# Kernel optimization log

Measured on AMD Instinct MI355X. Metric: run time of the kernel, lower is better.

The kernel has to match this reference:

```python
import jax, jax.numpy as jnp
import numpy as np

B, L, DIM, DQK = 4, 8192, 512, 512
THRESH = 0.5
TARGET_N = 6.0
RATIO_W = 0.03
LR_DIFF = 0.75
EPS = 1e-8


def setup_inputs() -> dict:
    key = jax.random.key(0)
    k1, k2, k3 = jax.random.split(key, 3)
    tokens = jax.random.normal(k1, (B, L, DIM), dtype=jnp.float32)
    # Linear(dim, 2*dqk, bias=False) weight, torch layout [out, in]
    Wqk = jax.random.normal(k2, (2 * DQK, DIM), dtype=jnp.float32) / np.sqrt(DIM).astype(np.float32)
    start_key = jax.random.normal(k3, (DQK,), dtype=jnp.float32) * 0.01  # heads=1
    return {"tokens": tokens, "Wqk": Wqk, "start_key": start_key}


def _straight_through(t, value):
    return t + jax.lax.stop_gradient(value - t)


def _frac_gradient(t, frac):
    # forward = t, backward grad scaled by frac
    return _straight_through(t * frac, t)


def _cosine_sim(a, b):
    dot = jnp.sum(a * b, axis=-1)
    na = jnp.maximum(jnp.sqrt(jnp.sum(a * a, axis=-1)), EPS)
    nb = jnp.maximum(jnp.sqrt(jnp.sum(b * b, axis=-1)), EPS)
    return dot / (na * nb)


def _assoc_scan(gates, x):
    # h_t = gates_t * h_{t-1} + x_t along axis 1 (inclusive first-order scan)
    def comb(l, r):
        al, bl = l
        ar, br = r
        return al * ar, br + ar * bl
    _, h = jax.lax.associative_scan(comb, (gates[..., None], x), axis=1)
    return h


def reference(tokens, Wqk, start_key):
    Bn, Ln, D = tokens.shape
    qk = jnp.einsum('bnd,ed->bne', tokens, Wqk)          # [B, L, 2*DQK]
    queries, keys = qk[..., :DQK], qk[..., DQK:]
    # key for position i is key_{i-1}, with learned start key at position 0
    keys_shift = jnp.concatenate(
        [jnp.broadcast_to(start_key, (Bn, 1, DQK)), keys[:, :-1]], axis=1)
    cos = _cosine_sim(queries, keys_shift)               # [B, L]
    probs = (1.0 - cos) * 0.5
    boundary = (probs > THRESH).at[:, 0].set(True)       # [B, L] bool
    num_chunks = boundary.sum(axis=-1)                   # [B]

    # stable compaction: boundary positions first, in order
    order = jnp.argsort(jnp.logical_not(boundary).astype(jnp.int32), axis=1)  # [B, L]
    ar = jnp.arange(Ln)
    chunk_mask = ar[None, :] < num_chunks[:, None]       # valid chunk slots
    pos = jnp.where(chunk_mask, order, Ln)               # boundary positions, sentinel L
    next_pos = jnp.concatenate([pos[:, 1:], jnp.full((Bn, 1), Ln, dtype=pos.dtype)], axis=1)
    chunk_lens = jnp.where(chunk_mask, next_pos - pos, 0)  # [B, L] int

    gathered = jnp.take_along_axis(tokens, order[..., None], axis=1)  # [B, L, D]
    boundary_probs = jnp.where(chunk_mask, jnp.take_along_axis(probs, order, axis=1), 0.0)
    gates = 1.0 - boundary_probs                         # padded slots -> 1 (matches torch, never read)
    downsampled = gathered * boundary_probs[..., None]   # padded slots -> 0

    confidence = jnp.where(boundary, probs, 1.0 - probs)
    scale = _straight_through(confidence, 1.0)           # forward value 1.0

    # aux ratio loss (with straight-through soft boundary fraction)
    Nt = TARGET_N
    F_hard = boundary.astype(probs.dtype)
    F_soft = jax.nn.sigmoid(probs - THRESH)
    F = _straight_through(F_soft, F_hard)
    Gm = probs.mean(axis=-1)
    Fm = F.mean(axis=-1)
    aux = (Nt / (Nt - 1.0)) * ((Nt - 1.0) * Fm * Gm + (1.0 - Fm) * (1.0 - Gm))
    weighted_aux_loss = aux.mean() * RATIO_W

    downsampled_out = _frac_gradient(downsampled, 1.0 / LR_DIFF)

    # ---- upsample path (the returned closure in the torch module) ----
    scanned = _assoc_scan(gates, downsampled_out)        # smooth across chunks
    rank = jnp.cumsum(boundary.astype(jnp.int32), axis=1) - 1  # chunk id of each token
    upsampled = jnp.take_along_axis(scanned, rank[..., None], axis=1)  # [B, L, D]
    upsampled = upsampled * scale[..., None]
    upsampled = _frac_gradient(upsampled, LR_DIFF)

    return downsampled_out, upsampled, weighted_aux_loss
```

## Files before the change

### kernel.cpp

```cpp
#include <hip/hip_runtime.h>
#include <cstdint>
#include <cstddef>

#define L 8192
#define BATCH 4
#define DQK 512
#define M_TOT (BATCH*L)
#define EPSC 1e-8f

typedef __attribute__((ext_vector_type(8))) short bf16x8;
typedef __attribute__((ext_vector_type(4))) float f32x4;
typedef __attribute__((ext_vector_type(8))) unsigned short u16x8;

__device__ __forceinline__ unsigned short bf16_rne(float x) {
  union { float f; unsigned u; } v; v.f = x;
  unsigned r = v.u + 0x7fffu + ((v.u >> 16) & 1u);
  return (unsigned short)(r >> 16);
}
__device__ __forceinline__ float bf16_tof(unsigned short b) {
  union { unsigned u; float f; } v; v.u = ((unsigned)b) << 16;
  return v.f;
}
__device__ __forceinline__ void gload_lds16(const void* g, void* l) {
  __builtin_amdgcn_global_load_lds(
      (const __attribute__((address_space(1))) unsigned int*)g,
      (__attribute__((address_space(3))) unsigned int*)l, 16, 0, 0);
}

__global__ __launch_bounds__(256) void k_split(const float* __restrict__ tokens,
                                               const float* __restrict__ Wqk,
                                               unsigned short* __restrict__ A1,
                                               unsigned short* __restrict__ A2,
                                               unsigned short* __restrict__ A3,
                                               unsigned short* __restrict__ W1,
                                               unsigned short* __restrict__ W2,
                                               unsigned short* __restrict__ W3) {
  const float* src; unsigned short *d1, *d2, *d3; size_t e0;
  if (blockIdx.x < 8192) {
    src = tokens; d1 = A1; d2 = A2; d3 = A3;
    e0 = ((size_t)blockIdx.x * 256 + threadIdx.x) * 8;
  } else {
    src = Wqk; d1 = W1; d2 = W2; d3 = W3;
    e0 = ((size_t)(blockIdx.x - 8192) * 256 + threadIdx.x) * 8;
  }
  float v[8];
  *(float4*)&v[0] = *(const float4*)(src + e0);
  *(float4*)&v[4] = *(const float4*)(src + e0 + 4);
  unsigned short o1[8], o2[8], o3[8];
  #pragma unroll
  for (int j = 0; j < 8; ++j) {
    float x = v[j];
    unsigned short b1 = bf16_rne(x);
    float r1 = x - bf16_tof(b1);
    unsigned short b2 = bf16_rne(r1);
    float r2 = r1 - bf16_tof(b2);
    unsigned short b3 = bf16_rne(r2);
    o1[j] = b1; o2[j] = b2; o3[j] = b3;
  }
  *(u16x8*)(d1 + e0) = *(u16x8*)o1;
  *(u16x8*)(d2 + e0) = *(u16x8*)o2;
  *(u16x8*)(d3 + e0) = *(u16x8*)o3;
}

__global__ __launch_bounds__(256, 3) void k_gemm_bf16(
    const unsigned short* __restrict__ A1, const unsigned short* __restrict__ A2,
    const unsigned short* __restrict__ A3,
    const unsigned short* __restrict__ W1, const unsigned short* __restrict__ W2,
    const unsigned short* __restrict__ W3,
    float* __restrict__ C) {
  __shared__ unsigned short lds[6 * 512 * 8];
  const int g = (blockIdx.x & 7) * 256 + (blockIdx.x >> 3);
  const int bx = g & 7;
  const int by = g >> 3;
  const int t = threadIdx.x;
  const int lane = t & 63;
  const int w = t >> 6;
  const int wr = w >> 1, wc = w & 1;

  f32x4 acc[4][4];
  #pragma unroll
  for (int i = 0; i < 4; ++i)
    #pragma unroll
    for (int j = 0; j < 4; ++j) acc[i][j] = (f32x4){0.f, 0.f, 0.f, 0.f};

  const unsigned short* srcA[3] = {A1, A2, A3};
  const unsigned short* srcW[3] = {W1, W2, W3};
  const int arow = by * 128;
  const int wrow = bx * 128;
  const int kg = lane >> 4;
  const int fr = lane & 15;

  for (int ks = 0; ks < 16; ++ks) {
    __syncthreads();
    const int kofs = ks * 32;
    #pragma unroll
    for (int s = 0; s < 3; ++s) {
      #pragma unroll
      for (int it = 0; it < 2; ++it) {
        const int p = it * 256 + t;
        const int row = p & 127, pg = p >> 7;
        gload_lds16(srcA[s] + (size_t)(arow + row) * 512 + kofs + pg * 8,
                    &lds[(s * 512 + p) * 8]);
        gload_lds16(srcW[s] + (size_t)(wrow + row) * 512 + kofs + pg * 8,
                    &lds[((3 + s) * 512 + p) * 8]);
      }
    }
    __syncthreads();

    bf16x8 bfr[4][3];
    #pragma unroll
    for (int nf = 0; nf < 4; ++nf) {
      const int row = wc * 64 + nf * 16 + fr;
      #pragma unroll
      for (int s = 0; s < 3; ++s)
        bfr[nf][s] = *(const bf16x8*)&lds[(((3 + s) * 512) + kg * 128 + row) * 8];
    }
    #pragma unroll
    for (int mf = 0; mf < 4; ++mf) {
      const int row = wr * 64 + mf * 16 + fr;
      bf16x8 a1 = *(const bf16x8*)&lds[((0 * 512) + kg * 128 + row) * 8];
      bf16x8 a2 = *(const bf16x8*)&lds[((1 * 512) + kg * 128 + row) * 8];
      bf16x8 a3 = *(const bf16x8*)&lds[((2 * 512) + kg * 128 + row) * 8];
      #pragma unroll
      for (int nf = 0; nf < 4; ++nf) {
        f32x4 c = acc[mf][nf];
        c = __builtin_amdgcn_mfma_f32_16x16x32_bf16(a1, bfr[nf][0], c, 0, 0, 0);
        c = __builtin_amdgcn_mfma_f32_16x16x32_bf16(a1, bfr[nf][1], c, 0, 0, 0);
        c = __builtin_amdgcn_mfma_f32_16x16x32_bf16(a2, bfr[nf][0], c, 0, 0, 0);
        c = __builtin_amdgcn_mfma_f32_16x16x32_bf16(a2, bfr[nf][1], c, 0, 0, 0);
        c = __builtin_amdgcn_mfma_f32_16x16x32_bf16(a1, bfr[nf][2], c, 0, 0, 0);
        c = __builtin_amdgcn_mfma_f32_16x16x32_bf16(a3, bfr[nf][0], c, 0, 0, 0);
        acc[mf][nf] = c;
      }
    }
  }
  const int fq = lane >> 4;
  #pragma unroll
  for (int mf = 0; mf < 4; ++mf) {
    #pragma unroll
    for (int nf = 0; nf < 4; ++nf) {
      const int col = bx * 128 + wc * 64 + nf * 16 + fr;
      #pragma unroll
      for (int r = 0; r < 4; ++r) {
        const int rrow = by * 128 + wr * 64 + mf * 16 + fq * 4 + r;
        C[(size_t)rrow * 1024 + col] = acc[mf][nf][r];
      }
    }
  }
}

__global__ __launch_bounds__(256) void k_gemm(const float* __restrict__ A,
                                              const float* __restrict__ W,
                                              float* __restrict__ C) {
  __shared__ float As[8][128];
  __shared__ float Bs[8][128];
  const int bx = blockIdx.x & 7;
  const int by = blockIdx.x >> 3;
  const int t  = threadIdx.x;
  const int tx = t & 15, ty = t >> 4;
  const int lr = t >> 1;
  const int lc = (t & 1) * 4;
  const float* Ag = A + (size_t)(by*128 + lr)*512 + lc;
  const float* Wg = W + (size_t)(bx*128 + lr)*512 + lc;
  float acc[8][8];
  #pragma unroll
  for (int i=0;i<8;i++)
    #pragma unroll
    for (int j=0;j<8;j++) acc[i][j]=0.f;

  for (int k0 = 0; k0 < 512; k0 += 8) {
    float4 av = *(const float4*)(Ag + k0);
    float4 bv = *(const float4*)(Wg + k0);
    __syncthreads();
    As[lc+0][lr]=av.x; As[lc+1][lr]=av.y; As[lc+2][lr]=av.z; As[lc+3][lr]=av.w;
    Bs[lc+0][lr]=bv.x; Bs[lc+1][lr]=bv.y; Bs[lc+2][lr]=bv.z; Bs[lc+3][lr]=bv.w;
    __syncthreads();
    #pragma unroll
    for (int kk=0;kk<8;kk++) {
      float af[8], bf[8];
      *(float4*)&af[0] = *(const float4*)&As[kk][ty*8];
      *(float4*)&af[4] = *(const float4*)&As[kk][ty*8+4];
      *(float4*)&bf[0] = *(const float4*)&Bs[kk][tx*8];
      *(float4*)&bf[4] = *(const float4*)&Bs[kk][tx*8+4];
      #pragma unroll
      for (int i=0;i<8;i++)
        #pragma unroll
        for (int j=0;j<8;j++)
          acc[i][j] = fmaf(af[i], bf[j], acc[i][j]);
    }
  }
  const int crow = by*128 + ty*8;
  const int ccol = bx*128 + tx*8;
  #pragma unroll
  for (int i=0;i<8;i++) {
    float* cp = C + (size_t)(crow+i)*1024 + ccol;
    *(float4*)cp     = make_float4(acc[i][0],acc[i][1],acc[i][2],acc[i][3]);
    *(float4*)(cp+4) = make_float4(acc[i][4],acc[i][5],acc[i][6],acc[i][7]);
  }
}

__global__ __launch_bounds__(256) void k_cos(const float* __restrict__ qk,
                                             const float* __restrict__ start_key,
                                             float* __restrict__ probs) {
  const int wid = threadIdx.x >> 6;
  const int lane = threadIdx.x & 63;
  const int p = blockIdx.x*4 + wid;
  const int n = p & (L-1);
  const float* q  = qk + (size_t)p*1024;
  const float* ks = (n==0) ? start_key : (qk + (size_t)(p-1)*1024 + 512);
  float dot=0.f, nq=0.f, nk=0.f;
  const int e0 = lane*8;
  #pragma unroll
  for (int j=0;j<8;j+=4) {
    float4 qv = *(const float4*)(q+e0+j);
    float4 kv = *(const float4*)(ks+e0+j);
    dot = fmaf(qv.x,kv.x,dot); dot = fmaf(qv.y,kv.y,dot);
    dot = fmaf(qv.z,kv.z,dot); dot = fmaf(qv.w,kv.w,dot);
    nq  = fmaf(qv.x,qv.x,nq);  nq  = fmaf(qv.y,qv.y,nq);
    nq  = fmaf(qv.z,qv.z,nq);  nq  = fmaf(qv.w,qv.w,nq);
    nk  = fmaf(kv.x,kv.x,nk);  nk  = fmaf(kv.y,kv.y,nk);
    nk  = fmaf(kv.z,kv.z,nk);  nk  = fmaf(kv.w,kv.w,nk);
  }
  #pragma unroll
  for (int m=32;m>=1;m>>=1) {
    dot += __shfl_xor(dot,m);
    nq  += __shfl_xor(nq,m);
    nk  += __shfl_xor(nk,m);
  }
  if (lane==0) {
    float na = fmaxf(sqrtf(nq), EPSC);
    float nb = fmaxf(sqrtf(nk), EPSC);
    float c  = dot/(na*nb);
    probs[p] = 0.5f*(1.f - c);
  }
}

__global__ __launch_bounds__(1024) void k_scan_bd(const float* __restrict__ probs,
                                                  int* __restrict__ bpos,
                                                  int* __restrict__ num_chunks,
                                                  float* __restrict__ auxvals) {
  const int b = blockIdx.x;
  const float* pb = probs + b*L;
  const int t = threadIdx.x;
  float pv[8]; int bd[8];
  const int base = t*8;
  float psum=0.f; int cnt=0;
  #pragma unroll
  for (int j=0;j<8;j++) {
    pv[j] = pb[base+j];
    bd[j] = (base+j == 0) || (pv[j] > 0.5f);
    cnt += bd[j];
    psum += pv[j];
  }
  const int lane = t & 63, w = t >> 6;
  int x = cnt;
  #pragma unroll
  for (int off=1; off<64; off<<=1) {
    int y = __shfl_up(x, off);
    if (lane >= off) x += y;
  }
  float ps = psum;
  #pragma unroll
  for (int m=32;m>=1;m>>=1) ps += __shfl_xor(ps, m);
  __shared__ int wsum[16]; __shared__ int wpre[17]; __shared__ float fsum[16];
  if (lane == 63) wsum[w] = x;
  if (lane == 0)  fsum[w] = ps;
  __syncthreads();
  if (t == 0) {
    int run = 0; float tot = 0.f;
    for (int i=0;i<16;i++) { wpre[i] = run; run += wsum[i]; tot += fsum[i]; }
    wpre[16] = run;
    num_chunks[b] = run;
    float Gm = tot / (float)L;
    float Fm = (float)run / (float)L;
    auxvals[b] = 1.2f * (5.f*Fm*Gm + (1.f-Fm)*(1.f-Gm));
  }
  __syncthreads();
  int rank = wpre[w] + (x - cnt);
  #pragma unroll
  for (int j=0;j<8;j++) {
    if (bd[j]) { bpos[b*L + rank] = base + j; rank++; }
  }
}

__global__ __launch_bounds__(512) void k_scan_local(const float* __restrict__ tokens,
                                                    const float* __restrict__ probs,
                                                    const int* __restrict__ bpos,
                                                    const int* __restrict__ num_chunks,
                                                    float* __restrict__ local_h,
                                                    float* __restrict__ gpref,
                                                    float* __restrict__ hend,
                                                    float* __restrict__ Pseg,
                                                    float* __restrict__ down) {
  const int b = blockIdx.x >> 6;
  const int s = blockIdx.x & 63;
  const int c = threadIdx.x;
  const int nc = num_chunks[b];
  const int i0 = s*128;
  const int seg = b*64 + s;
  const int z0 = (i0 > nc) ? i0 : nc;
  for (int i = z0; i < i0 + 128; ++i)
    down[((size_t)(b*L + i))*512 + c] = 0.f;
  if (i0 >= nc) {
    hend[(size_t)seg*512 + c] = 0.f;
    if (c==0) Pseg[seg] = 1.f;
    return;
  }
  const int iend = (i0+128 < nc) ? i0+128 : nc;
  const int cntc = iend - i0;
  __shared__ float p_s[128];
  __shared__ int n_s[128];
  if (c < cntc) {
    int n = bpos[b*L + i0 + c];
    n_s[c] = n;
    p_s[c] = probs[b*L + n];
  }
  __syncthreads();
  float h = 0.f, gp = 1.f;
  for (int i = i0; i < iend; ++i) {
    const int ii = i - i0;
    const float p = p_s[ii];
    const float g = 1.f - p;
    const float x = tokens[((size_t)(b*L + n_s[ii]))*512 + c] * p;
    h = fmaf(g, h, x);
    gp *= g;
    down[((size_t)(b*L + i))*512 + c] = x;
    local_h[((size_t)(b*L + i))*512 + c] = h;
    if (c==0) gpref[b*L + i] = gp;
  }
  hend[(size_t)seg*512 + c] = h;
  if (c==0) Pseg[seg] = gp;
}

__global__ __launch_bounds__(512) void k_seg_combine(const float* __restrict__ hend,
                                                     const float* __restrict__ Pseg,
                                                     float* __restrict__ carry_in) {
  const int b = blockIdx.x;
  const int c = threadIdx.x;
  float carry = 0.f;
  for (int s = 0; s < 64; ++s) {
    const int seg = b*64 + s;
    carry_in[(size_t)seg*512 + c] = carry;
    carry = fmaf(Pseg[seg], carry, hend[(size_t)seg*512 + c]);
  }
}

__global__ __launch_bounds__(512) void k_expand(const float* __restrict__ local_h,
                                                const float* __restrict__ gpref,
                                                const float* __restrict__ carry_in,
                                                const int* __restrict__ bpos,
                                                const int* __restrict__ num_chunks,
                                                float* __restrict__ up) {
  const int b = blockIdx.x >> 6;
  const int s = blockIdx.x & 63;
  const int c = threadIdx.x;
  const int nc = num_chunks[b];
  const int i0 = s*128;
  if (i0 >= nc) return;
  const int iend = (i0+128 < nc) ? i0+128 : nc;
  const int cntc = iend - i0;
  __shared__ int n_s[129];
  __shared__ float gp_s[128];
  if (c < cntc) { n_s[c] = bpos[b*L + i0 + c]; gp_s[c] = gpref[b*L + i0 + c]; }
  if (c == 0)   n_s[cntc] = (iend < nc) ? bpos[b*L + iend] : L;
  __syncthreads();
  const float carry = carry_in[((size_t)(b*64 + s))*512 + c];
  for (int i = i0; i < iend; ++i) {
    const int ii = i - i0;
    const float hf = fmaf(gp_s[ii], carry, local_h[((size_t)(b*L + i))*512 + c]);
    const int n0 = n_s[ii], n1 = n_s[ii+1];
    for (int n = n0; n < n1; ++n)
      up[((size_t)(b*L + n))*512 + c] = hf;
  }
}

__global__ void k_final(const float* __restrict__ auxvals, float* __restrict__ outp) {
  outp[0] = (auxvals[0]+auxvals[1]+auxvals[2]+auxvals[3]) * 0.25f * 0.03f;
}

extern "C" void kernel_launch(void* const* d_in, const int* in_sizes, int n_in,
                              void* d_out, int out_size, void* d_ws, size_t ws_size,
                              hipStream_t stream) {
  const float* tokens    = (const float*)d_in[0];
  const float* Wqk       = (const float*)d_in[1];
  const float* start_key = (const float*)d_in[2];
  float* out  = (float*)d_out;
  float* down = out;
  float* up   = out + (size_t)M_TOT*512;
  float* qk   = out;

  char* ws = (char*)d_ws;
  const size_t A_BYTES = (size_t)M_TOT*512*2;
  const size_t W_BYTES = (size_t)1024*512*2;
  const size_t STAGED_BASE = 3*A_BYTES + 3*W_BYTES;
  const size_t SMALL_BYTES = (size_t)M_TOT*4*3 + (size_t)BATCH*64*512*4*2
                           + (size_t)BATCH*64*4 + BATCH*4*2 + 256;
  const bool staged = ws_size >= STAGED_BASE + SMALL_BYTES;

  unsigned short* A1 = (unsigned short*)ws;
  unsigned short* A2 = (unsigned short*)(ws + A_BYTES);
  unsigned short* A3 = (unsigned short*)(ws + 2*A_BYTES);
  unsigned short* W1 = (unsigned short*)(ws + 3*A_BYTES);
  unsigned short* W2 = (unsigned short*)(ws + 3*A_BYTES + W_BYTES);
  unsigned short* W3 = (unsigned short*)(ws + 3*A_BYTES + 2*W_BYTES);

  float* local_h = (float*)ws;
  size_t off = staged ? STAGED_BASE : (size_t)M_TOT*512*4;
  float* probs    = (float*)(ws + off); off += (size_t)M_TOT*4;
  int*   bpos     = (int*)  (ws + off); off += (size_t)M_TOT*4;
  float* gpref    = (float*)(ws + off); off += (size_t)M_TOT*4;
  float* hend     = (float*)(ws + off); off += (size_t)BATCH*64*512*4;
  float* carry_in = (float*)(ws + off); off += (size_t)BATCH*64*512*4;
  float* Pseg     = (float*)(ws + off); off += (size_t)BATCH*64*4;
  int*   num_chunks = (int*)(ws + off); off += (size_t)BATCH*4;
  float* auxvals  = (float*)(ws + off); off += (size_t)BATCH*4;

  if (staged) {
    k_split<<<8448, 256, 0, stream>>>(tokens, Wqk, A1, A2, A3, W1, W2, W3);
    k_gemm_bf16<<<2048, 256, 0, stream>>>(A1, A2, A3, W1, W2, W3, qk);
  } else {
    k_gemm<<<2048, 256, 0, stream>>>(tokens, Wqk, qk);
  }
  k_cos<<<M_TOT/4, 256, 0, stream>>>(qk, start_key, probs);
  k_scan_bd<<<BATCH, 1024, 0, stream>>>(probs, bpos, num_chunks, auxvals);
  k_scan_local<<<BATCH*64, 512, 0, stream>>>(tokens, probs, bpos, num_chunks,
                                             local_h, gpref, hend, Pseg, down);
  k_seg_combine<<<BATCH, 512, 0, stream>>>(hend, Pseg, carry_in);
  k_expand<<<BATCH*64, 512, 0, stream>>>(local_h, gpref, carry_in, bpos, num_chunks, up);
  k_final<<<1, 1, 0, stream>>>(auxvals, out + (size_t)2*M_TOT*512);
}
```

Measured before the change: 411.4 us.

## Recompute local scan in expand instead of storing local_h; parallel segment carry scan

The local scan kernel no longer writes the per-position local_h and gpref arrays. The expand kernel instead rescans each segment from its carry-in, re-reading down and probs. The serial per-batch segment combine is replaced by a parallel Hillis-Steele scan over segments, and segments shrink from 128 to 64 chunks so there are twice as many blocks. This removes a full [B,L,512] write and re-read of local_h, at the cost of re-reading down, a serial recurrence inside expand, and some extra memory traffic for the larger hend/carry arrays.

```diff
diff --git a/kernel.cpp b/kernel.cpp
--- a/kernel.cpp
+++ b/kernel.cpp
@@ -6,6 +6,8 @@
 #define BATCH 4
 #define DQK 512
 #define M_TOT (BATCH*L)
+#define NSEG 128
+#define SEGC 64
 #define EPSC 1e-8f
 
 typedef __attribute__((ext_vector_type(8))) short bf16x8;
@@ -287,29 +289,27 @@
                                                     const float* __restrict__ probs,
                                                     const int* __restrict__ bpos,
                                                     const int* __restrict__ num_chunks,
-                                                    float* __restrict__ local_h,
-                                                    float* __restrict__ gpref,
                                                     float* __restrict__ hend,
                                                     float* __restrict__ Pseg,
                                                     float* __restrict__ down) {
-  const int b = blockIdx.x >> 6;
-  const int s = blockIdx.x & 63;
+  const int b = blockIdx.x / NSEG;
+  const int s = blockIdx.x - b * NSEG;
   const int c = threadIdx.x;
   const int nc = num_chunks[b];
-  const int i0 = s*128;
-  const int seg = b*64 + s;
+  const int i0 = s*SEGC;
+  const int seg = b*NSEG + s;
   const int z0 = (i0 > nc) ? i0 : nc;
-  for (int i = z0; i < i0 + 128; ++i)
+  for (int i = z0; i < i0 + SEGC; ++i)
     down[((size_t)(b*L + i))*512 + c] = 0.f;
   if (i0 >= nc) {
     hend[(size_t)seg*512 + c] = 0.f;
     if (c==0) Pseg[seg] = 1.f;
     return;
   }
-  const int iend = (i0+128 < nc) ? i0+128 : nc;
+  const int iend = (i0+SEGC < nc) ? i0+SEGC : nc;
   const int cntc = iend - i0;
-  __shared__ float p_s[128];
-  __shared__ int n_s[128];
+  __shared__ float p_s[SEGC];
+  __shared__ int n_s[SEGC];
   if (c < cntc) {
     int n = bpos[b*L + i0 + c];
     n_s[c] = n;
@@ -325,52 +325,71 @@
     h = fmaf(g, h, x);
     gp *= g;
     down[((size_t)(b*L + i))*512 + c] = x;
-    local_h[((size_t)(b*L + i))*512 + c] = h;
-    if (c==0) gpref[b*L + i] = gp;
   }
   hend[(size_t)seg*512 + c] = h;
   if (c==0) Pseg[seg] = gp;
 }
 
-__global__ __launch_bounds__(512) void k_seg_combine(const float* __restrict__ hend,
-                                                     const float* __restrict__ Pseg,
-                                                     float* __restrict__ carry_in) {
-  const int b = blockIdx.x;
-  const int c = threadIdx.x;
-  float carry = 0.f;
-  for (int s = 0; s < 64; ++s) {
-    const int seg = b*64 + s;
-    carry_in[(size_t)seg*512 + c] = carry;
-    carry = fmaf(Pseg[seg], carry, hend[(size_t)seg*512 + c]);
-  }
-}
-
-__global__ __launch_bounds__(512) void k_expand(const float* __restrict__ local_h,
-                                                const float* __restrict__ gpref,
-                                                const float* __restrict__ carry_in,
+__global__ __launch_bounds__(512) void k_seg_scan(const float* __restrict__ hend,
+                                                  const float* __restrict__ Pseg,
+                                                  float* __restrict__ carry_in) {
+  const int b   = blockIdx.x >> 7;
+  const int gch = blockIdx.x & 127;
+  const int sg  = threadIdx.x & 127;
+  const int cl  = threadIdx.x >> 7;
+  const int ch  = gch*4 + cl;
+  const int seg = b*NSEG + sg;
+  float h = hend[(size_t)seg*512 + ch];
+  float P = Pseg[seg];
+  __shared__ float sh[512], sP[512];
+  const int idx = cl*128 + sg;
+  #pragma unroll
+  for (int off=1; off<NSEG; off<<=1) {
+    sh[idx] = h; sP[idx] = P;
+    __syncthreads();
+    if (sg >= off) {
+      h = fmaf(P, sh[idx-off], h);
+      P = P * sP[idx-off];
+    }
+    __syncthreads();
+  }
+  sh[idx] = h;
+  __syncthreads();
+  carry_in[(size_t)seg*512 + ch] = (sg==0) ? 0.f : sh[idx-1];
+}
+
+__global__ __launch_bounds__(512) void k_expand(const float* __restrict__ down,
+                                                const float* __restrict__ probs,
                                                 const int* __restrict__ bpos,
                                                 const int* __restrict__ num_chunks,
+                                                const float* __restrict__ carry_in,
                                                 float* __restrict__ up) {
-  const int b = blockIdx.x >> 6;
-  const int s = blockIdx.x & 63;
+  const int b = blockIdx.x / NSEG;
+  const int s = blockIdx.x - b * NSEG;
   const int c = threadIdx.x;
   const int nc = num_chunks[b];
-  const int i0 = s*128;
+  const int i0 = s*SEGC;
   if (i0 >= nc) return;
-  const int iend = (i0+128 < nc) ? i0+128 : nc;
+  const int iend = (i0+SEGC < nc) ? i0+SEGC : nc;
   const int cntc = iend - i0;
-  __shared__ int n_s[129];
-  __shared__ float gp_s[128];
-  if (c < cntc) { n_s[c] = bpos[b*L + i0 + c]; gp_s[c] = gpref[b*L + i0 + c]; }
+  __shared__ float p_s[SEGC];
+  __shared__ int n_s[SEGC+1];
+  if (c < cntc) {
+    int n = bpos[b*L + i0 + c];
+    n_s[c] = n;
+    p_s[c] = probs[b*L + n];
+  }
   if (c == 0)   n_s[cntc] = (iend < nc) ? bpos[b*L + iend] : L;
   __syncthreads();
-  const float carry = carry_in[((size_t)(b*64 + s))*512 + c];
+  float h = carry_in[((size_t)(b*NSEG + s))*512 + c];
   for (int i = i0; i < iend; ++i) {
     const int ii = i - i0;
-    const float hf = fmaf(gp_s[ii], carry, local_h[((size_t)(b*L + i))*512 + c]);
+    const float g = 1.f - p_s[ii];
+    const float x = down[((size_t)(b*L + i))*512 + c];
+    h = fmaf(g, h, x);
     const int n0 = n_s[ii], n1 = n_s[ii+1];
     for (int n = n0; n < n1; ++n)
-      up[((size_t)(b*L + n))*512 + c] = hf;
+      up[((size_t)(b*L + n))*512 + c] = h;
   }
 }
 
@@ -393,8 +412,8 @@
   const size_t A_BYTES = (size_t)M_TOT*512*2;
   const size_t W_BYTES = (size_t)1024*512*2;
   const size_t STAGED_BASE = 3*A_BYTES + 3*W_BYTES;
-  const size_t SMALL_BYTES = (size_t)M_TOT*4*3 + (size_t)BATCH*64*512*4*2
-                           + (size_t)BATCH*64*4 + BATCH*4*2 + 256;
+  const size_t SMALL_BYTES = (size_t)M_TOT*4*2 + (size_t)BATCH*NSEG*512*4*2
+                           + (size_t)BATCH*NSEG*4 + BATCH*4*2 + 256;
   const bool staged = ws_size >= STAGED_BASE + SMALL_BYTES;
 
   unsigned short* A1 = (unsigned short*)ws;
@@ -404,14 +423,12 @@
   unsigned short* W2 = (unsigned short*)(ws + 3*A_BYTES + W_BYTES);
   unsigned short* W3 = (unsigned short*)(ws + 3*A_BYTES + 2*W_BYTES);
 
-  float* local_h = (float*)ws;
-  size_t off = staged ? STAGED_BASE : (size_t)M_TOT*512*4;
+  size_t off = staged ? STAGED_BASE : 0;
   float* probs    = (float*)(ws + off); off += (size_t)M_TOT*4;
   int*   bpos     = (int*)  (ws + off); off += (size_t)M_TOT*4;
-  float* gpref    = (float*)(ws + off); off += (size_t)M_TOT*4;
-  float* hend     = (float*)(ws + off); off += (size_t)BATCH*64*512*4;
-  float* carry_in = (float*)(ws + off); off += (size_t)BATCH*64*512*4;
-  float* Pseg     = (float*)(ws + off); off += (size_t)BATCH*64*4;
+  float* hend     = (float*)(ws + off); off += (size_t)BATCH*NSEG*512*4;
+  float* carry_in = (float*)(ws + off); off += (size_t)BATCH*NSEG*512*4;
+  float* Pseg     = (float*)(ws + off); off += (size_t)BATCH*NSEG*4;
   int*   num_chunks = (int*)(ws + off); off += (size_t)BATCH*4;
   float* auxvals  = (float*)(ws + off); off += (size_t)BATCH*4;
 
@@ -423,9 +440,9 @@
   }
   k_cos<<<M_TOT/4, 256, 0, stream>>>(qk, start_key, probs);
   k_scan_bd<<<BATCH, 1024, 0, stream>>>(probs, bpos, num_chunks, auxvals);
-  k_scan_local<<<BATCH*64, 512, 0, stream>>>(tokens, probs, bpos, num_chunks,
-                                             local_h, gpref, hend, Pseg, down);
-  k_seg_combine<<<BATCH, 512, 0, stream>>>(hend, Pseg, carry_in);
-  k_expand<<<BATCH*64, 512, 0, stream>>>(local_h, gpref, carry_in, bpos, num_chunks, up);
+  k_scan_local<<<BATCH*NSEG, 512, 0, stream>>>(tokens, probs, bpos, num_chunks,
+                                               hend, Pseg, down);
+  k_seg_scan<<<BATCH*NSEG, 512, 0, stream>>>(hend, Pseg, carry_in);
+  k_expand<<<BATCH*NSEG, 512, 0, stream>>>(down, probs, bpos, num_chunks, carry_in, up);
   k_final<<<1, 1, 0, stream>>>(auxvals, out + (size_t)2*M_TOT*512);
 }
```

After: 368.6 us. -10.4%, faster.
